# Kernel tuning notes

Measured on AMD Instinct MI355X. Metric: run time of the kernel, lower is better.

The kernel has to match this reference:

```python
import jax, jax.numpy as jnp
import numpy as np

N = 60000          # users
M = 40000          # items
NODES = N + M
D = 64             # embedding_dim
NLAYERS = 3        # layers = [64, 64, 64]
NNZ = 3_200_000    # nnz of L_I (avg degree 32)
B = 1024           # batch_size
NEG_SLOPE = 0.2


def setup_inputs() -> dict:
    key = jax.random.key(0)
    ks = jax.random.split(key, 12)
    edge_row = jax.random.randint(ks[0], (NNZ,), 0, NODES, dtype=jnp.int32)
    edge_col = jax.random.randint(ks[1], (NNZ,), 0, NODES, dtype=jnp.int32)
    # Laplacian values are small positive normalized weights
    edge_val = jax.random.uniform(ks[2], (NNZ,), dtype=jnp.float32) * (1.0 / 32.0)
    embed_user = jax.random.normal(ks[3], (N, D), dtype=jnp.float32) * 0.1
    embed_item = jax.random.normal(ks[4], (M, D), dtype=jnp.float32) * 0.1
    W1 = jax.random.normal(ks[5], (NLAYERS, D, D), dtype=jnp.float32) * 0.1
    W2 = jax.random.normal(ks[6], (NLAYERS, D, D), dtype=jnp.float32) * 0.1
    b1 = jax.random.normal(ks[7], (NLAYERS, 1, D), dtype=jnp.float32) * 0.1
    b2 = jax.random.normal(ks[8], (NLAYERS, 1, D), dtype=jnp.float32) * 0.1
    sampled_users = jax.random.randint(ks[9], (B,), 0, N, dtype=jnp.int32)
    observed_items_idx = jax.random.randint(ks[10], (B,), 0, M, dtype=jnp.int32)
    unobserved_items_idx = jax.random.randint(ks[11], (B,), 0, M, dtype=jnp.int32)
    return {
        "edge_row": edge_row, "edge_col": edge_col, "edge_val": edge_val,
        "embed_user": embed_user, "embed_item": embed_item,
        "W1": W1, "W2": W2, "b1": b1, "b2": b2,
        "sampled_users": sampled_users,
        "observed_items_idx": observed_items_idx,
        "unobserved_items_idx": unobserved_items_idx,
    }


def _spmm(row, col, val, x):
    # sparse (NODES x NODES) @ dense (NODES x D) via gather + segment-sum
    return jax.ops.segment_sum(val[:, None] * x[col], row, num_segments=NODES)


def reference(edge_row, edge_col, edge_val, embed_user, embed_item,
              W1, W2, b1, b2,
              sampled_users, observed_items_idx, unobserved_items_idx):
    x = jnp.concatenate([embed_user, embed_item], axis=0)  # (NODES, D)
    reprs = [x]
    for i in range(NLAYERS):
        lie = _spmm(edge_row, edge_col, edge_val, x)        # L_I @ E
        left = lie @ W1[i] + b1[i]
        right = (x * lie) @ W2[i] + b2[i]
        x = jax.nn.leaky_relu(left + right, negative_slope=NEG_SLOPE)
        reprs.append(x)
    final_reprs = jnp.concatenate(reprs, axis=1)            # (NODES, D*(NLAYERS+1))
    users_, items_ = final_reprs[:N], final_reprs[N:]
    return (users_[sampled_users],
            items_[observed_items_idx],
            items_[unobserved_items_idx])
```

## Files before the change

### kernel.cpp

```cpp
#include <hip/hip_runtime.h>

#define NN    60000
#define NODES 100000
#define DD    64
#define NNZ   3200000
#define BB    1024
#define NEG   0.2f
#define RPB   196
#define NBUCK 511
#define EPB   8192
#define NPB   ((NNZ + EPB - 1) / EPB)
#define CAP   7000
#define BCAP  7168
#define NSEG  13
#define KEYN  (NSEG * RPB)
#define SPB   (KEYN + 1)

__global__ __launch_bounds__(256) void k_init_x(const float* __restrict__ eu,
                                                const float* __restrict__ ei,
                                                float* __restrict__ x,
                                                int* __restrict__ gcur) {
    int i = blockIdx.x * 256 + threadIdx.x;
    if (i < NBUCK) gcur[i] = i * CAP;
    const int TOT = NODES * DD / 4;
    if (i >= TOT) return;
    const int UE = NN * DD / 4;
    float4 v = (i < UE) ? ((const float4*)eu)[i] : ((const float4*)ei)[i - UE];
    ((float4*)x)[i] = v;
}

__global__ __launch_bounds__(512) void k_place(const int* __restrict__ row,
                                               const int* __restrict__ col,
                                               const float* __restrict__ val,
                                               int* __restrict__ gcur,
                                               int2* __restrict__ bulk) {
    __shared__ int rows_l[EPB];
    __shared__ unsigned short perm[EPB];
    __shared__ int h[NBUCK], bloc[NBUCK], bcur[NBUCK], gseg[NBUCK];
    __shared__ int sc[512];
    int t = threadIdx.x;
    if (t < NBUCK) h[t] = 0;
    __syncthreads();
    int base = blockIdx.x * EPB;
    int n = min(EPB, NNZ - base);
    for (int k = t; k < n; k += 512) {
        int r = row[base + k];
        rows_l[k] = r;
        atomicAdd(&h[r / RPB], 1);
    }
    __syncthreads();
    {
        int v = (t < NBUCK) ? h[t] : 0;
        sc[t] = v;
        __syncthreads();
        for (int off = 1; off < 512; off <<= 1) {
            int u = (t >= off) ? sc[t - off] : 0;
            __syncthreads();
            sc[t] += u;
            __syncthreads();
        }
        if (t < NBUCK) {
            int ex = sc[t] - v;
            bloc[t] = ex;
            bcur[t] = ex;
            gseg[t] = v ? atomicAdd(&gcur[t], v) : 0;
        }
    }
    __syncthreads();
    for (int k = t; k < n; k += 512) {
        int p = atomicAdd(&bcur[rows_l[k] / RPB], 1);
        perm[p] = (unsigned short)k;
    }
    __syncthreads();
    for (int j = t; j < n; j += 512) {
        int k = perm[j];
        int r = rows_l[k];
        int b = r / RPB;
        int addr = gseg[b] + (j - bloc[b]);
        bulk[addr] = make_int2(((r - b * RPB) << 17) | col[base + k],
                               __float_as_int(val[base + k]));
    }
}

__global__ __launch_bounds__(512) void k_csr(const int* __restrict__ gcur,
                                             int2* __restrict__ bulk,
                                             int* __restrict__ starts) {
    __shared__ int2 eds[BCAP];
    __shared__ int cnt[KEYN], pos[KEYN];
    __shared__ int part[512];
    int b = blockIdx.x, t = threadIdx.x;
    int lo = b * CAP;
    int n = gcur[b] - lo;
    for (int k = t; k < KEYN; k += 512) cnt[k] = 0;
    __syncthreads();
    for (int i = t; i < n; i += 512) {
        int2 ed = bulk[lo + i];
        eds[i] = ed;
        int lr = ed.x >> 17, c = ed.x & 0x1FFFF;
        atomicAdd(&cnt[(c >> 13) * RPB + lr], 1);
    }
    __syncthreads();
    int run = 0;
#pragma unroll
    for (int j = 0; j < 5; ++j) {
        int k = t * 5 + j;
        if (k < KEYN) { pos[k] = run; run += cnt[k]; }
    }
    part[t] = run;
    __syncthreads();
    for (int off = 1; off < 512; off <<= 1) {
        int u = (t >= off) ? part[t - off] : 0;
        __syncthreads();
        part[t] += u;
        __syncthreads();
    }
    int poff = part[t] - run;
#pragma unroll
    for (int j = 0; j < 5; ++j) {
        int k = t * 5 + j;
        if (k < KEYN) pos[k] += poff;
    }
    __syncthreads();
    for (int k = t; k < KEYN; k += 512) {
        starts[b * SPB + k] = lo + pos[k];
        cnt[k] = pos[k];
    }
    if (t == 0) starts[b * SPB + KEYN] = lo + n;
    __syncthreads();
    for (int i = t; i < n; i += 512) {
        int2 ed = eds[i];
        int lr = ed.x >> 17, c = ed.x & 0x1FFFF;
        int p = atomicAdd(&cnt[(c >> 13) * RPB + lr], 1);
        bulk[lo + p] = ed;
    }
}

__global__ __launch_bounds__(1024) void k_cspmm(const int* __restrict__ starts,
                                                const int2* __restrict__ cv,
                                                const float* __restrict__ x,
                                                float* __restrict__ lie) {
    __shared__ float acc[RPB * DD];
    int t = threadIdx.x, b = blockIdx.x;
    float4* av = (float4*)acc;
    for (int i = t; i < RPB * 16; i += 1024) av[i] = make_float4(0.f, 0.f, 0.f, 0.f);
    __syncthreads();
    int lane = t & 63;
    int wid = __builtin_amdgcn_readfirstlane(t >> 6);
    int r0 = (wid * RPB) >> 4;
    int r1 = ((wid + 1) * RPB) >> 4;
    int sb = b * SPB;
    for (int seg = 0; seg < NSEG; ++seg) {
        int s = starts[sb + seg * RPB + r0];
        int e = starts[sb + seg * RPB + r1];
        if (s >= e) continue;
        int cur = -1;
        float f = 0.f;
        int2 nxt = cv[s + lane];
        for (int base = s; base < e; base += 64) {
            int2 cb = nxt;
            if (base + 64 < e) nxt = cv[base + 64 + lane];
            int cnt = min(64, e - base);
            for (int j0 = 0; j0 < cnt; j0 += 8) {
                int   sx[8];
                float vv[8];
                float xg[8];
#pragma unroll
                for (int j = 0; j < 8; ++j) {
                    int jj = j0 + j;
                    int jc = (jj < cnt) ? jj : (cnt - 1);
                    int ex = __builtin_amdgcn_readlane(cb.x, jc);
                    int ey = __builtin_amdgcn_readlane(cb.y, jc);
                    sx[j] = ex;
                    vv[j] = (jj < cnt) ? __int_as_float(ey) : 0.f;
                    xg[j] = x[(ex & 0x1FFFF) * DD + lane];
                }
#pragma unroll
                for (int j = 0; j < 8; ++j) {
                    int r = ((unsigned)sx[j]) >> 17;
                    if (r != cur) {
                        if (cur >= 0) acc[cur * DD + lane] += f;
                        cur = r; f = 0.f;
                    }
                    f = fmaf(vv[j], xg[j], f);
                }
            }
        }
        if (cur >= 0) acc[cur * DD + lane] += f;
    }
    __syncthreads();
    int row0 = b * RPB;
    for (int i = t; i < RPB * 16; i += 1024) {
        int gr = row0 + (i >> 4);
        if (gr < NODES) ((float4*)lie)[gr * 16 + (i & 15)] = av[i];
    }
}

__global__ __launch_bounds__(256) void k_gemm(float* __restrict__ x,
                                              const float* __restrict__ lie,
                                              const float* __restrict__ W1,
                                              const float* __restrict__ W2,
                                              const float* __restrict__ b1,
                                              const float* __restrict__ b2) {
    __shared__ float A1[64 * 64];
    __shared__ float A2[64 * 64];
    __shared__ float Ws1[64 * 64];
    __shared__ float Ws2[64 * 64];

    const int t = threadIdx.x;
    const int row0 = blockIdx.x * 64;

    {
        const float4* w1v = (const float4*)W1;
        const float4* w2v = (const float4*)W2;
        float4* s1v = (float4*)Ws1;
        float4* s2v = (float4*)Ws2;
#pragma unroll
        for (int q = 0; q < 4; ++q) {
            s1v[q * 256 + t] = w1v[q * 256 + t];
            s2v[q * 256 + t] = w2v[q * 256 + t];
        }
    }
#pragma unroll
    for (int q = 0; q < 4; ++q) {
        int f4 = q * 256 + t;
        int rl = f4 >> 4;
        int c4 = f4 & 15;
        int gr = row0 + rl;
        float4 lv = make_float4(0.f, 0.f, 0.f, 0.f);
        float4 xv = make_float4(0.f, 0.f, 0.f, 0.f);
        if (gr < NODES) {
            lv = *(const float4*)&lie[gr * DD + c4 * 4];
            xv = *(const float4*)&x[gr * DD + c4 * 4];
        }
        int sg = c4 ^ (rl & 15);
        ((float4*)A1)[rl * 16 + sg] = lv;
        ((float4*)A2)[rl * 16 + sg] = make_float4(lv.x * xv.x, lv.y * xv.y,
                                                  lv.z * xv.z, lv.w * xv.w);
    }
    __syncthreads();

    const int tx = t & 15;
    const int ty = t >> 4;
    float bs[4];
    {
        float4 bb1 = *(const float4*)&b1[tx * 4];
        float4 bb2 = *(const float4*)&b2[tx * 4];
        bs[0] = bb1.x + bb2.x; bs[1] = bb1.y + bb2.y;
        bs[2] = bb1.z + bb2.z; bs[3] = bb1.w + bb2.w;
    }
    float acc[4][4];
#pragma unroll
    for (int i = 0; i < 4; ++i)
#pragma unroll
        for (int j = 0; j < 4; ++j) acc[i][j] = bs[j];

    for (int k4 = 0; k4 < 16; ++k4) {
        float4 a1[4], a2[4];
#pragma unroll
        for (int i = 0; i < 4; ++i) {
            int r = ty * 4 + i;
            int sg = k4 ^ (r & 15);
            a1[i] = ((const float4*)A1)[r * 16 + sg];
            a2[i] = ((const float4*)A2)[r * 16 + sg];
        }
#pragma unroll
        for (int kk = 0; kk < 4; ++kk) {
            float4 w1 = ((const float4*)Ws1)[(k4 * 4 + kk) * 16 + tx];
            float4 w2 = ((const float4*)Ws2)[(k4 * 4 + kk) * 16 + tx];
#pragma unroll
            for (int i = 0; i < 4; ++i) {
                float av1 = (&a1[i].x)[kk];
                float av2 = (&a2[i].x)[kk];
                acc[i][0] = fmaf(av1, w1.x, fmaf(av2, w2.x, acc[i][0]));
                acc[i][1] = fmaf(av1, w1.y, fmaf(av2, w2.y, acc[i][1]));
                acc[i][2] = fmaf(av1, w1.z, fmaf(av2, w2.z, acc[i][2]));
                acc[i][3] = fmaf(av1, w1.w, fmaf(av2, w2.w, acc[i][3]));
            }
        }
    }
#pragma unroll
    for (int i = 0; i < 4; ++i) {
        int gr = row0 + ty * 4 + i;
        if (gr < NODES) {
            float4 o;
            o.x = acc[i][0] >= 0.f ? acc[i][0] : NEG * acc[i][0];
            o.y = acc[i][1] >= 0.f ? acc[i][1] : NEG * acc[i][1];
            o.z = acc[i][2] >= 0.f ? acc[i][2] : NEG * acc[i][2];
            o.w = acc[i][3] >= 0.f ? acc[i][3] : NEG * acc[i][3];
            *(float4*)&x[gr * DD + tx * 4] = o;
        }
    }
}

__global__ __launch_bounds__(256) void k_gather(const float* __restrict__ x,
                                                const int* __restrict__ su,
                                                const int* __restrict__ oi,
                                                const int* __restrict__ ui,
                                                float* __restrict__ out, int layer) {
    int w    = (blockIdx.x * 256 + threadIdx.x) >> 6;
    int lane = threadIdx.x & 63;
    if (w >= 3 * BB) return;
    int g = w >> 10, b = w & 1023;
    int node = (g == 0) ? su[b] : (NN + ((g == 1) ? oi[b] : ui[b]));
    out[w * 256 + layer * 64 + lane] = x[node * DD + lane];
}

extern "C" void kernel_launch(void* const* d_in, const int* in_sizes, int n_in,
                              void* d_out, int out_size, void* d_ws, size_t ws_size,
                              hipStream_t stream) {
    const int*   edge_row = (const int*)d_in[0];
    const int*   edge_col = (const int*)d_in[1];
    const float* edge_val = (const float*)d_in[2];
    const float* eu = (const float*)d_in[3];
    const float* ei = (const float*)d_in[4];
    const float* W1 = (const float*)d_in[5];
    const float* W2 = (const float*)d_in[6];
    const float* b1 = (const float*)d_in[7];
    const float* b2 = (const float*)d_in[8];
    const int*   su = (const int*)d_in[9];
    const int*   oi = (const int*)d_in[10];
    const int*   ui = (const int*)d_in[11];
    float* out = (float*)d_out;

    float* x      = (float*)d_ws;
    float* lie    = x + NODES * DD;
    int2*  bulk   = (int2*)(lie + NODES * DD);
    int*   gcur   = (int*)(bulk + NBUCK * CAP);
    int*   starts = gcur + NBUCK + 1;

    k_init_x<<<(NODES * DD / 4 + 255) / 256, 256, 0, stream>>>(eu, ei, x, gcur);
    k_gather<<<(3 * BB * 64 + 255) / 256, 256, 0, stream>>>(x, su, oi, ui, out, 0);

    k_place<<<NPB, 512, 0, stream>>>(edge_row, edge_col, edge_val, gcur, bulk);
    k_csr<<<NBUCK, 512, 0, stream>>>(gcur, bulk, starts);

    for (int l = 0; l < 3; ++l) {
        k_cspmm<<<NBUCK, 1024, 0, stream>>>(starts, bulk, x, lie);
        k_gemm<<<(NODES + 63) / 64, 256, 0, stream>>>(x, lie,
                                                      W1 + l * 4096, W2 + l * 4096,
                                                      b1 + l * 64,  b2 + l * 64);
        k_gather<<<(3 * BB * 64 + 255) / 256, 256, 0, stream>>>(x, su, oi, ui, out, l + 1);
    }
}
```

Measured before the change: 585.0 us.

## Double-buffer edge segments in LDS and software-pipeline gathers in SpMM

The SpMM kernel now stages each column segment's edges into a double-buffered shared-memory array, prefetching the next segment into registers while the current one is processed. The inner loop is rewritten so that blocks of 16 x-row gathers alternate between two register sets, keeping more loads in flight before the accumulation step. The goal is to hide global-memory latency on edge metadata and gathers. The cost is two block-wide barriers per segment, more shared memory and registers, and a fixed 1792-edge cap per segment that silently drops edges if a segment is larger.

```diff
diff --git a/kernel.cpp b/kernel.cpp
--- a/kernel.cpp
+++ b/kernel.cpp
@@ -15,6 +15,8 @@
 #define NSEG  13
 #define KEYN  (NSEG * RPB)
 #define SPB   (KEYN + 1)
+#define ESEG  1792
+#define BLK   16
 
 __global__ __launch_bounds__(256) void k_init_x(const float* __restrict__ eu,
                                                 const float* __restrict__ ei,
@@ -140,52 +142,78 @@
                                                 const float* __restrict__ x,
                                                 float* __restrict__ lie) {
     __shared__ float acc[RPB * DD];
+    __shared__ int2 eb[2][ESEG];
     int t = threadIdx.x, b = blockIdx.x;
     float4* av = (float4*)acc;
     for (int i = t; i < RPB * 16; i += 1024) av[i] = make_float4(0.f, 0.f, 0.f, 0.f);
-    __syncthreads();
     int lane = t & 63;
     int wid = __builtin_amdgcn_readfirstlane(t >> 6);
     int r0 = (wid * RPB) >> 4;
     int r1 = ((wid + 1) * RPB) >> 4;
     int sb = b * SPB;
+
+    {
+        int g0 = starts[sb];
+        int g1 = starts[sb + RPB];
+        int n0 = g1 - g0; if (n0 > ESEG) n0 = ESEG;
+        for (int i = t; i < n0; i += 1024) eb[0][i] = cv[g0 + i];
+    }
+    __syncthreads();
+
     for (int seg = 0; seg < NSEG; ++seg) {
-        int s = starts[sb + seg * RPB + r0];
-        int e = starts[sb + seg * RPB + r1];
-        if (s >= e) continue;
-        int cur = -1;
-        float f = 0.f;
-        int2 nxt = cv[s + lane];
-        for (int base = s; base < e; base += 64) {
-            int2 cb = nxt;
-            if (base + 64 < e) nxt = cv[base + 64 + lane];
-            int cnt = min(64, e - base);
-            for (int j0 = 0; j0 < cnt; j0 += 8) {
-                int   sx[8];
-                float vv[8];
-                float xg[8];
-#pragma unroll
-                for (int j = 0; j < 8; ++j) {
-                    int jj = j0 + j;
-                    int jc = (jj < cnt) ? jj : (cnt - 1);
-                    int ex = __builtin_amdgcn_readlane(cb.x, jc);
-                    int ey = __builtin_amdgcn_readlane(cb.y, jc);
-                    sx[j] = ex;
-                    vv[j] = (jj < cnt) ? __int_as_float(ey) : 0.f;
-                    xg[j] = x[(ex & 0x1FFFF) * DD + lane];
-                }
-#pragma unroll
-                for (int j = 0; j < 8; ++j) {
-                    int r = ((unsigned)sx[j]) >> 17;
-                    if (r != cur) {
-                        if (cur >= 0) acc[cur * DD + lane] += f;
-                        cur = r; f = 0.f;
-                    }
-                    f = fmaf(vv[j], xg[j], f);
-                }
+        int nn = 0; int2 stgA, stgB;
+        if (seg + 1 < NSEG) {
+            int s1 = starts[sb + (seg + 1) * RPB];
+            int e1 = starts[sb + (seg + 2) * RPB];
+            nn = e1 - s1; if (nn > ESEG) nn = ESEG;
+            if (t < nn) stgA = cv[s1 + t];
+            if (t + 1024 < nn) stgB = cv[s1 + t + 1024];
+        }
+        const int2* ep = eb[seg & 1];
+        int segb = starts[sb + seg * RPB];
+        int sA = starts[sb + seg * RPB + r0] - segb;
+        int eA = starts[sb + seg * RPB + r1] - segb;
+        if (eA > ESEG) eA = ESEG;
+        if (sA > eA) sA = eA;
+        if (sA < eA) {
+            int cur = -1; float f = 0.f;
+            int sx0[BLK], sx1[BLK];
+            float vv0[BLK], vv1[BLK], xg0[BLK], xg1[BLK];
+            int i = sA;
+#define LOADB(S, base_) { \
+    _Pragma("unroll") \
+    for (int j = 0; j < BLK; ++j) { \
+        int idx = (base_) + j; \
+        int idc = idx < eA ? idx : eA - 1; \
+        int2 ed = ep[idc]; \
+        int ex = __builtin_amdgcn_readfirstlane(ed.x); \
+        int ey = __builtin_amdgcn_readfirstlane(ed.y); \
+        sx##S[j] = ex; \
+        vv##S[j] = (idx < eA) ? __int_as_float(ey) : 0.f; \
+        xg##S[j] = x[(ex & 0x1FFFF) * DD + lane]; \
+    } }
+#define CONSB(S) { \
+    _Pragma("unroll") \
+    for (int j = 0; j < BLK; ++j) { \
+        int r = ((unsigned)sx##S[j]) >> 17; \
+        if (r != cur) { if (cur >= 0) acc[cur * DD + lane] += f; cur = r; f = 0.f; } \
+        f = fmaf(vv##S[j], xg##S[j], f); \
+    } }
+            LOADB(0, i)
+            for (;;) {
+                if (i + BLK < eA) { LOADB(1, i + BLK) CONSB(0) i += BLK; }
+                else             { CONSB(0) break; }
+                if (i + BLK < eA) { LOADB(0, i + BLK) CONSB(1) i += BLK; }
+                else             { CONSB(1) break; }
             }
-        }
-        if (cur >= 0) acc[cur * DD + lane] += f;
+            if (cur >= 0) acc[cur * DD + lane] += f;
+#undef LOADB
+#undef CONSB
+        }
+        __syncthreads();
+        if (t < nn) eb[(seg & 1) ^ 1][t] = stgA;
+        if (t + 1024 < nn) eb[(seg & 1) ^ 1][t + 1024] = stgB;
+        __syncthreads();
     }
     __syncthreads();
     int row0 = b * RPB;
```

Measured after the change: 734.4 us. 1.26x slower.
